# Performance work log

Hardware: AMD Instinct MI355X
Metric: run time of the kernel (lower is better)

The kernel has to match this reference:

```python
import jax, jax.numpy as jnp
import numpy as np


def _proj(x, W, b):
    # 1x1 conv == per-pixel dense: [B,H,W,Cin] @ [Cin,Cout] + [Cout]
    return jnp.einsum('bhwc,cd->bhwd', x, W) + b


def setup_inputs() -> dict:
    key = jax.random.key(0)
    ks = jax.random.split(key, 5)
    B, Wd, Hd, C = 8, 64, 64, 128
    scale = 1.0 / np.sqrt(C)
    inp = {'x': jax.random.normal(ks[0], (B, Wd, Hd, C), dtype=jnp.float32)}
    for i, name in enumerate(['f', 'g', 'h', 'v']):
        inp['W' + name] = jax.random.normal(ks[i + 1], (C, C), dtype=jnp.float32) * scale
        inp['b' + name] = jnp.zeros((C,), dtype=jnp.float32)
    return inp


def reference(x, Wf, bf, Wg, bg, Wh, bh, Wv, bv):
    B, W, H, C = x.shape
    N = W * H
    fx = _proj(x, Wf, bf).reshape(B, N, C)
    gx = _proj(x, Wg, bg).reshape(B, N, C)
    hx = _proj(x, Wh, bh).reshape(B, N, C)
    # alpha[b,n,m] = softmax over m of fx @ gx^T
    alpha = jax.nn.softmax(jnp.einsum('bnc,bmc->bnm', fx, gx), axis=-1)
    # o = hx^T @ alpha -> [B, C, N], then reshape to [B, W, H, C] (faithful to original)
    o = jnp.einsum('bnc,bnm->bcm', hx, alpha).reshape(B, W, H, C)
    return _proj(o, Wv, bv)
```

## Files before the change

kernel.cpp:

```cpp
#include <hip/hip_runtime.h>
#include <math.h>

#define NB 8
#define NN 4096
#define NC 128

typedef __attribute__((ext_vector_type(8)))  short bf16x8;
typedef __attribute__((ext_vector_type(4)))  float f32x4;
typedef __attribute__((ext_vector_type(16))) float f32x16;

#define L2E   1.4426950408889634f
#define SBIAS 43.2808512266689f

static __device__ __forceinline__ float fexp2(float x) { return __builtin_amdgcn_exp2f(x); }
static __device__ __forceinline__ float flog2(float x) { return __builtin_amdgcn_logf(x); }

static __device__ __forceinline__ unsigned short f2bf(float f) {
    unsigned u = __builtin_bit_cast(unsigned, f);
    return (unsigned short)((u + 0x7FFFu + ((u >> 16) & 1u)) >> 16);
}


__global__ __launch_bounds__(256) void k_proj(
    const float* __restrict__ x,
    const float* __restrict__ Wf, const float* __restrict__ bf,
    const float* __restrict__ Wg, const float* __restrict__ bg,
    const float* __restrict__ Wh, const float* __restrict__ bh,
    unsigned short* __restrict__ fb, unsigned short* __restrict__ gb,
    unsigned short* __restrict__ htb)
{
    const float* W; const float* bias;
    if (blockIdx.z == 0)      { W = Wf; bias = bf; }
    else if (blockIdx.z == 1) { W = Wg; bias = bg; }
    else                      { W = Wh; bias = bh; }

    __shared__ __align__(16) float ast[32 * 32];
    __shared__ __align__(16) float bs [32 * 128];

    const int tid = threadIdx.x;
    const int tx = tid & 31, ty = tid >> 5;
    const int r0 = blockIdx.x * 32;

    float acc[4][4] = {};

    for (int cc = 0; cc < 128; cc += 32) {
        __syncthreads();
        {
            int r = tid >> 3, c4 = tid & 7;
            float4 v = *(const float4*)&x[(size_t)(r0 + r) * NC + cc + c4 * 4];
            ast[(c4 * 4 + 0) * 32 + r] = v.x;
            ast[(c4 * 4 + 1) * 32 + r] = v.y;
            ast[(c4 * 4 + 2) * 32 + r] = v.z;
            ast[(c4 * 4 + 3) * 32 + r] = v.w;
        }
        #pragma unroll
        for (int i = 0; i < 4; i++) {
            int idx = tid + i * 256;
            *(float4*)&bs[idx * 4] = *(const float4*)&W[(size_t)cc * 128 + idx * 4];
        }
        __syncthreads();
        #pragma unroll
        for (int c = 0; c < 32; c++) {
            float4 a  = *(const float4*)&ast[c * 32 + ty * 4];
            float4 b4 = *(const float4*)&bs [c * 128 + tx * 4];
            acc[0][0] += a.x * b4.x; acc[0][1] += a.x * b4.y; acc[0][2] += a.x * b4.z; acc[0][3] += a.x * b4.w;
            acc[1][0] += a.y * b4.x; acc[1][1] += a.y * b4.y; acc[1][2] += a.y * b4.z; acc[1][3] += a.y * b4.w;
            acc[2][0] += a.z * b4.x; acc[2][1] += a.z * b4.y; acc[2][2] += a.z * b4.z; acc[2][3] += a.z * b4.w;
            acc[3][0] += a.w * b4.x; acc[3][1] += a.w * b4.y; acc[3][2] += a.w * b4.z; acc[3][3] += a.w * b4.w;
        }
    }

    float4 bb = *(const float4*)&bias[tx * 4];
    float bbv[4] = { bb.x, bb.y, bb.z, bb.w };

    if (blockIdx.z < 2) {
        unsigned short* out = (blockIdx.z == 0) ? fb : gb;
        const int kc = tx >> 2, hi2 = (tx >> 1) & 1, j0 = (tx & 1) * 4;
        const size_t base = ((size_t)(r0 >> 5) * 8 + kc) * 512;
        #pragma unroll
        for (int i = 0; i < 4; i++) {
            ushort4 v;
            v.x = f2bf(acc[i][0] + bbv[0]);
            v.y = f2bf(acc[i][1] + bbv[1]);
            v.z = f2bf(acc[i][2] + bbv[2]);
            v.w = f2bf(acc[i][3] + bbv[3]);
            int lane = (ty * 4 + i) + 32 * hi2;
            *(ushort4*)&out[base + (size_t)lane * 8 + j0] = v;
        }
    } else {
        const int b   = r0 >> 12;
        const int ncc = (r0 & (NN - 1)) >> 5;
        const int s   = ty >> 2, hj = (ty >> 1) & 1, jj0 = (ty & 1) * 4;
        const int cb  = tx >> 3;
        #pragma unroll
        for (int j = 0; j < 4; j++) {
            int c = tx * 4 + j;
            int lane = (c & 31) + 32 * hj;
            ushort4 v;
            v.x = f2bf(acc[0][j] + bbv[j]);
            v.y = f2bf(acc[1][j] + bbv[j]);
            v.z = f2bf(acc[2][j] + bbv[j]);
            v.w = f2bf(acc[3][j] + bbv[j]);
            size_t off = ((((size_t)(b * 4 + cb) * 128 + ncc) * 2 + s) * 64 + lane) * 8 + jj0;
            *(ushort4*)&htb[off] = v;
        }
    }
}

__global__ __launch_bounds__(512, 2) void k_stats(
    const unsigned short* __restrict__ fb, const unsigned short* __restrict__ gb,
    float* __restrict__ Cout)
{
    const int b = blockIdx.y;
    const int tid = threadIdx.x;
    const int w = tid >> 6;
    const int l = tid & 63;
    const int t = w & 1, q = w >> 1;
    const int nbase = blockIdx.x * 64 + t * 32;

    const size_t fbase = ((size_t)(b * 128 + (nbase >> 5)) * 8) * 512 + (size_t)l * 8;
    bf16x8 bfr[8];
    #pragma unroll
    for (int kc = 0; kc < 8; kc++)
        bfr[kc] = *(const bf16x8*)&fb[fbase + kc * 512];

    float sum = 0.f;
    for (int mt = 0; mt < 32; mt += 2) {
        const size_t gbaseA = ((size_t)(b * 128 + q * 32 + mt) * 8) * 512 + (size_t)l * 8;
        const size_t gbaseB = gbaseA + 8 * 512;
        f32x16 S0A = {}; f32x16 S1A = {};
        f32x16 S0B = {}; f32x16 S1B = {};
        #pragma unroll
        for (int kc = 0; kc < 8; kc += 2) {
            S0A = __builtin_amdgcn_mfma_f32_32x32x16_bf16(*(const bf16x8*)&gb[gbaseA + kc * 512], bfr[kc], S0A, 0, 0, 0);
            S1A = __builtin_amdgcn_mfma_f32_32x32x16_bf16(*(const bf16x8*)&gb[gbaseA + (kc + 1) * 512], bfr[kc + 1], S1A, 0, 0, 0);
            S0B = __builtin_amdgcn_mfma_f32_32x32x16_bf16(*(const bf16x8*)&gb[gbaseB + kc * 512], bfr[kc], S0B, 0, 0, 0);
            S1B = __builtin_amdgcn_mfma_f32_32x32x16_bf16(*(const bf16x8*)&gb[gbaseB + (kc + 1) * 512], bfr[kc + 1], S1B, 0, 0, 0);
        }
        #pragma unroll
        for (int r = 0; r < 16; r++)
            sum += fexp2(__builtin_fmaf(S0A[r] + S1A[r], L2E, -SBIAS));
        #pragma unroll
        for (int r = 0; r < 16; r++)
            sum += fexp2(__builtin_fmaf(S0B[r] + S1B[r], L2E, -SBIAS));
    }

    sum += __shfl_xor(sum, 32, 64);

    __shared__ float red[8][32];
    if (l < 32) red[w][l] = sum;
    __syncthreads();
    if (q == 0 && l < 32) {
        float tot = red[t][l] + red[t + 2][l] + red[t + 4][l] + red[t + 6][l];
        Cout[(size_t)b * NN + nbase + l] = -(SBIAS + flog2(tot));
    }
}

__global__ __launch_bounds__(512, 2) void k_out(
    const unsigned short* __restrict__ fb, const unsigned short* __restrict__ gb,
    const unsigned short* __restrict__ htb, const float* __restrict__ Cn,
    float* __restrict__ O0, float* __restrict__ O1, float* __restrict__ O2,
    float* __restrict__ Od, int nsplit)
{
    const int b = blockIdx.z;
    const int tid = threadIdx.x;
    const int w = tid >> 6, l = tid & 63;
    const int lr = l & 31, hi = l >> 5;
    const int m0 = blockIdx.x * 256 + w * 32;

    __shared__ __align__(16) char ldsF[2][8192];
    __shared__ __align__(16) char ldsH[2][8192];

    const int chunks = (NN / 32) / nsplit;
    const int c0g = blockIdx.y * chunks;
    float* O = Od;
    if ((int)blockIdx.y + 1 < nsplit)
        O = (blockIdx.y == 0) ? O0 : ((blockIdx.y == 1) ? O1 : O2);

    const size_t gbase = ((size_t)(b * 128 + blockIdx.x * 8 + w) * 8) * 512 + (size_t)l * 8;
    bf16x8 gfr[8];
    #pragma unroll
    for (int kc = 0; kc < 8; kc++)
        gfr[kc] = *(const bf16x8*)&gb[gbase + kc * 512];

    const float* Cb = Cn + (size_t)b * NN;

    const size_t fstage0 = (size_t)b * 128 * 4096 + (size_t)tid * 8;
    const int p = tid >> 6, pcb = p >> 1, ps = p & 1;
    const size_t hstage0 = ((size_t)(b * 4 + pcb) * 256 + ps) * 512 + (size_t)(tid & 63) * 8;

    f32x16 acc[4] = { {}, {}, {}, {} };

    uint4 fv = *(const uint4*)&fb[fstage0 + (size_t)c0g * 4096];
    uint4 hv = *(const uint4*)&htb[hstage0 + (size_t)c0g * 1024];

    for (int nc = 0; nc < chunks; nc++) {
        const int cur = nc & 1;
        const int ncg = c0g + nc;
        const int n0 = ncg * 32;
        const int ncgN = c0g + ((nc + 1 < chunks) ? nc + 1 : nc);

        *(uint4*)(ldsF[cur] + tid * 16) = fv;
        *(uint4*)(ldsH[cur] + tid * 16) = hv;
        __syncthreads();

        fv = *(const uint4*)&fb[fstage0 + (size_t)ncgN * 4096];
        hv = *(const uint4*)&htb[hstage0 + (size_t)ncgN * 1024];

        bf16x8 fcur[8];
        #pragma unroll
        for (int kc = 0; kc < 8; kc++)
            fcur[kc] = *(const bf16x8*)(ldsF[cur] + kc * 1024 + l * 16);

        bf16x8 hA[8];
        #pragma unroll
        for (int cb = 0; cb < 4; cb++) {
            hA[2 * cb]     = *(const bf16x8*)(ldsH[cur] + (cb * 2 + 0) * 1024 + l * 16);
            hA[2 * cb + 1] = *(const bf16x8*)(ldsH[cur] + (cb * 2 + 1) * 1024 + l * 16);
        }
        float4 Cv[4];
        #pragma unroll
        for (int q = 0; q < 4; q++)
            Cv[q] = *(const float4*)&Cb[n0 + q * 8 + hi * 4];

        f32x16 S0 = {}; f32x16 S1 = {};
        #pragma unroll
        for (int kc = 0; kc < 8; kc += 2) {
            S0 = __builtin_amdgcn_mfma_f32_32x32x16_bf16(fcur[kc], gfr[kc], S0, 0, 0, 0);
            S1 = __builtin_amdgcn_mfma_f32_32x32x16_bf16(fcur[kc + 1], gfr[kc + 1], S1, 0, 0, 0);
        }

        unsigned pk[8];
        #pragma unroll
        for (int pp = 0; pp < 8; pp++) {
            int r0i = 2 * pp, r1i = 2 * pp + 1;
            float a0 = fexp2(__builtin_fmaf(S0[r0i] + S1[r0i], L2E, Cv[r0i >> 2][r0i & 3]));
            float a1 = fexp2(__builtin_fmaf(S0[r1i] + S1[r1i], L2E, Cv[r1i >> 2][r1i & 3]));
            asm("v_cvt_pk_bf16_f32 %0, %1, %2" : "=v"(pk[pp]) : "v"(a0), "v"(a1));
        }

        asm("v_permlane32_swap_b32 %0, %1" : "+v"(pk[0]), "+v"(pk[2]));
        asm("v_permlane32_swap_b32 %0, %1" : "+v"(pk[1]), "+v"(pk[3]));
        asm("v_permlane32_swap_b32 %0, %1" : "+v"(pk[4]), "+v"(pk[6]));
        asm("v_permlane32_swap_b32 %0, %1" : "+v"(pk[5]), "+v"(pk[7]));
        uint4 b0, b1;
        b0.x = pk[0]; b0.y = pk[1]; b0.z = pk[2]; b0.w = pk[3];
        b1.x = pk[4]; b1.y = pk[5]; b1.z = pk[6]; b1.w = pk[7];
        bf16x8 B0 = __builtin_bit_cast(bf16x8, b0);
        bf16x8 B1 = __builtin_bit_cast(bf16x8, b1);

        #pragma unroll
        for (int cb = 0; cb < 4; cb++) {
            acc[cb] = __builtin_amdgcn_mfma_f32_32x32x16_bf16(hA[2 * cb],     B0, acc[cb], 0, 0, 0);
            acc[cb] = __builtin_amdgcn_mfma_f32_32x32x16_bf16(hA[2 * cb + 1], B1, acc[cb], 0, 0, 0);
        }
    }

    #pragma unroll
    for (int cb = 0; cb < 4; cb++) {
        #pragma unroll
        for (int r = 0; r < 16; r++) {
            int row = (r & 3) + 8 * (r >> 2) + 4 * hi;
            O[((size_t)b * NC + cb * 32 + row) * NN + m0 + lr] = acc[cb][r];
        }
    }
}

__global__ __launch_bounds__(256) void k_vproj(
    float* __restrict__ o, const float* __restrict__ E0,
    const float* __restrict__ E1, const float* __restrict__ E2,
    const float* __restrict__ Wv, const float* __restrict__ bv, int nextra)
{
    __shared__ __align__(16) float ast[32 * 32];
    __shared__ __align__(16) float bs [32 * 128];

    const int tid = threadIdx.x;
    const int tx = tid & 31, ty = tid >> 5;
    const int r0 = blockIdx.x * 32;

    float acc[4][4] = {};

    for (int cc = 0; cc < 128; cc += 32) {
        __syncthreads();
        {
            int r = tid >> 3, c4 = tid & 7;
            size_t idx = (size_t)(r0 + r) * NC + cc + c4 * 4;
            float4 v = *(const float4*)&o[idx];
            if (nextra > 0) {
                float4 u = *(const float4*)&E0[idx];
                v.x += u.x; v.y += u.y; v.z += u.z; v.w += u.w;
            }
            if (nextra > 1) {
                float4 u = *(const float4*)&E1[idx];
                v.x += u.x; v.y += u.y; v.z += u.z; v.w += u.w;
            }
            if (nextra > 2) {
                float4 u = *(const float4*)&E2[idx];
                v.x += u.x; v.y += u.y; v.z += u.z; v.w += u.w;
            }
            ast[(c4 * 4 + 0) * 32 + r] = v.x;
            ast[(c4 * 4 + 1) * 32 + r] = v.y;
            ast[(c4 * 4 + 2) * 32 + r] = v.z;
            ast[(c4 * 4 + 3) * 32 + r] = v.w;
        }
        #pragma unroll
        for (int i = 0; i < 4; i++) {
            int idx = tid + i * 256;
            *(float4*)&bs[idx * 4] = *(const float4*)&Wv[(size_t)cc * 128 + idx * 4];
        }
        __syncthreads();
        #pragma unroll
        for (int c = 0; c < 32; c++) {
            float4 a  = *(const float4*)&ast[c * 32 + ty * 4];
            float4 b4 = *(const float4*)&bs [c * 128 + tx * 4];
            acc[0][0] += a.x * b4.x; acc[0][1] += a.x * b4.y; acc[0][2] += a.x * b4.z; acc[0][3] += a.x * b4.w;
            acc[1][0] += a.y * b4.x; acc[1][1] += a.y * b4.y; acc[1][2] += a.y * b4.z; acc[1][3] += a.y * b4.w;
            acc[2][0] += a.z * b4.x; acc[2][1] += a.z * b4.y; acc[2][2] += a.z * b4.z; acc[2][3] += a.z * b4.w;
            acc[3][0] += a.w * b4.x; acc[3][1] += a.w * b4.y; acc[3][2] += a.w * b4.z; acc[3][3] += a.w * b4.w;
        }
    }
    float4 bb = *(const float4*)&bv[tx * 4];
    #pragma unroll
    for (int i = 0; i < 4; i++) {
        float4 r;
        r.x = acc[i][0] + bb.x; r.y = acc[i][1] + bb.y;
        r.z = acc[i][2] + bb.z; r.w = acc[i][3] + bb.w;
        *(float4*)&o[(size_t)(r0 + ty * 4 + i) * NC + tx * 4] = r;
    }
}

extern "C" void kernel_launch(void* const* d_in, const int* in_sizes, int n_in,
                              void* d_out, int out_size, void* d_ws, size_t ws_size,
                              hipStream_t stream)
{
    const float* x  = (const float*)d_in[0];
    const float* Wf = (const float*)d_in[1];
    const float* bf = (const float*)d_in[2];
    const float* Wg = (const float*)d_in[3];
    const float* bg = (const float*)d_in[4];
    const float* Wh = (const float*)d_in[5];
    const float* bh = (const float*)d_in[6];
    const float* Wv = (const float*)d_in[7];
    const float* bv = (const float*)d_in[8];
    float* out = (float*)d_out;

    unsigned short* fbp = (unsigned short*)d_ws;
    unsigned short* gbp = fbp + (size_t)NB * NN * NC;
    unsigned short* htp = gbp + (size_t)NB * NN * NC;
    float* Cn = (float*)(htp + (size_t)NB * NN * NC);
    float* Opart = Cn + (size_t)NB * NN;
    const size_t osz = (size_t)NB * NC * NN;
    size_t base = (size_t)((char*)Opart - (char*)d_ws);
    int nsplit = (ws_size >= base + osz * 4) ? 2 : 1;
    float* O0 = Opart;
    float* O1 = Opart + osz;
    float* O2 = Opart + 2 * osz;

    k_proj<<<dim3(1024, 1, 3), 256, 0, stream>>>(x, Wf, bf, Wg, bg, Wh, bh, fbp, gbp, htp);

    k_stats<<<dim3(NN / 64, NB), 512, 0, stream>>>(fbp, gbp, Cn);

    k_out<<<dim3(NN / 256, nsplit, NB), 512, 0, stream>>>(fbp, gbp, htp, Cn, O0, O1, O2, out, nsplit);

    k_vproj<<<dim3(1024), 256, 0, stream>>>(out, O0, O1, O2, Wv, bv, nsplit - 1);
}
```

Measured before the change: 215.9 us.

## Stage g tiles through double-buffered LDS in stats kernel to share across waves

In k_stats, each block now cooperatively loads the g tiles for all four q-groups into a double-buffered shared-memory buffer, with a register prefetch of the next tile. The two t-waves that previously loaded the same g data separately from global memory now share it through LDS, which halves global/L2 traffic for g. It adds one block-wide barrier per iteration and 64KB of LDS, which may limit occupancy below the requested 2 blocks per CU. It also wraps the MFMA section in s_setprio.

```diff
diff --git a/kernel.cpp b/kernel.cpp
--- a/kernel.cpp
+++ b/kernel.cpp
@@ -118,36 +118,55 @@
     const int t = w & 1, q = w >> 1;
     const int nbase = blockIdx.x * 64 + t * 32;
 
+    __shared__ __align__(16) char sg[2][4][8192];
+    __shared__ float red[8][32];
+
     const size_t fbase = ((size_t)(b * 128 + (nbase >> 5)) * 8) * 512 + (size_t)l * 8;
     bf16x8 bfr[8];
     #pragma unroll
     for (int kc = 0; kc < 8; kc++)
         bfr[kc] = *(const bf16x8*)&fb[fbase + kc * 512];
 
+    const int tq = tid >> 7, si = tid & 127;
+    const unsigned short* gsrc = gb + (size_t)(b * 128 + tq * 32) * 4096 + (size_t)si * 8;
+
+    uint4 pv[4];
+    #pragma unroll
+    for (int k = 0; k < 4; k++)
+        pv[k] = *(const uint4*)&gsrc[(size_t)k * 1024];
+
     float sum = 0.f;
-    for (int mt = 0; mt < 32; mt += 2) {
-        const size_t gbaseA = ((size_t)(b * 128 + q * 32 + mt) * 8) * 512 + (size_t)l * 8;
-        const size_t gbaseB = gbaseA + 8 * 512;
-        f32x16 S0A = {}; f32x16 S1A = {};
-        f32x16 S0B = {}; f32x16 S1B = {};
+    for (int mt = 0; mt < 32; mt++) {
+        const int cur = mt & 1;
+        char* dst = sg[cur][tq];
+        #pragma unroll
+        for (int k = 0; k < 4; k++)
+            *(uint4*)(dst + si * 16 + k * 2048) = pv[k];
+        __syncthreads();
+
+        const int mtn = (mt + 1 < 32) ? mt + 1 : mt;
+        #pragma unroll
+        for (int k = 0; k < 4; k++)
+            pv[k] = *(const uint4*)&gsrc[(size_t)mtn * 4096 + (size_t)k * 1024];
+
+        const char* gt = sg[cur][q];
+        __builtin_amdgcn_s_setprio(1);
+        f32x16 S0 = {}; f32x16 S1 = {};
         #pragma unroll
         for (int kc = 0; kc < 8; kc += 2) {
-            S0A = __builtin_amdgcn_mfma_f32_32x32x16_bf16(*(const bf16x8*)&gb[gbaseA + kc * 512], bfr[kc], S0A, 0, 0, 0);
-            S1A = __builtin_amdgcn_mfma_f32_32x32x16_bf16(*(const bf16x8*)&gb[gbaseA + (kc + 1) * 512], bfr[kc + 1], S1A, 0, 0, 0);
-            S0B = __builtin_amdgcn_mfma_f32_32x32x16_bf16(*(const bf16x8*)&gb[gbaseB + kc * 512], bfr[kc], S0B, 0, 0, 0);
-            S1B = __builtin_amdgcn_mfma_f32_32x32x16_bf16(*(const bf16x8*)&gb[gbaseB + (kc + 1) * 512], bfr[kc + 1], S1B, 0, 0, 0);
-        }
+            bf16x8 a0 = *(const bf16x8*)(gt + kc * 1024 + l * 16);
+            bf16x8 a1 = *(const bf16x8*)(gt + (kc + 1) * 1024 + l * 16);
+            S0 = __builtin_amdgcn_mfma_f32_32x32x16_bf16(a0, bfr[kc], S0, 0, 0, 0);
+            S1 = __builtin_amdgcn_mfma_f32_32x32x16_bf16(a1, bfr[kc + 1], S1, 0, 0, 0);
+        }
+        __builtin_amdgcn_s_setprio(0);
         #pragma unroll
         for (int r = 0; r < 16; r++)
-            sum += fexp2(__builtin_fmaf(S0A[r] + S1A[r], L2E, -SBIAS));
-        #pragma unroll
-        for (int r = 0; r < 16; r++)
-            sum += fexp2(__builtin_fmaf(S0B[r] + S1B[r], L2E, -SBIAS));
+            sum += fexp2(__builtin_fmaf(S0[r] + S1[r], L2E, -SBIAS));
     }
 
     sum += __shfl_xor(sum, 32, 64);
 
-    __shared__ float red[8][32];
     if (l < 32) red[w][l] = sum;
     __syncthreads();
     if (q == 0 && l < 32) {
```

After: 305.5 us. 41.5% more time.
